# Kernel optimization log

Hardware: AMD Instinct MI355X
Metric: run time of the kernel (lower is better)

## Reference

```python
import jax, jax.numpy as jnp
import numpy as np

N, D, H, K = 131072, 512, 128, 3
NPOS, NNEG = 8192, 8192
KM_ITERS = 4
PROTO_SHIFT = 0.15
PROTO_LOGIT_SCALE = 0.2
TEMP = 2.5


def _sq_cdist(x, c):
    # squared euclidean distance, matches torch.cdist(...).pow(2)
    d = jnp.sum(x * x, -1, keepdims=True) + jnp.sum(c * c, -1)[None, :] - 2.0 * (x @ c.T)
    return jnp.maximum(d, 0.0)


def _kmeans(x, k, iters):
    # torch.linspace(0, n-1, steps=k).long() init, fixed iteration count
    n = x.shape[0]
    idx = jnp.linspace(0.0, n - 1, k).astype(jnp.int32)
    centers = x[idx]
    for _ in range(iters):
        assign = jnp.argmin(_sq_cdist(x, centers), axis=1)
        sums = jax.ops.segment_sum(x, assign, num_segments=k)
        counts = jax.ops.segment_sum(jnp.ones((n,), x.dtype), assign, num_segments=k)[:, None]
        # empty cluster keeps old center (mask.any() branch in torch)
        centers = jnp.where(counts > 0, sums / jnp.maximum(counts, 1.0), centers)
    return centers


def setup_inputs() -> dict:
    key = jax.random.key(0)
    ks = jax.random.split(key, 10)
    s = 1.0 / np.sqrt(D).astype(np.float32)
    return {
        "z_cls": jax.random.normal(ks[0], (N, D), jnp.float32),
        "z_proto": jax.random.normal(ks[1], (N, D), jnp.float32),
        "pos_ctx": jax.random.normal(ks[2], (D,), jnp.float32),
        "neg_ctx": jax.random.normal(ks[3], (D,), jnp.float32),
        "W1": jax.random.normal(ks[4], (H, D), jnp.float32) * s,
        "b1": jnp.zeros((H,), jnp.float32),
        "W2": jax.random.normal(ks[5], (1, H), jnp.float32) * (1.0 / np.sqrt(H).astype(np.float32)),
        "b2": jnp.zeros((1,), jnp.float32),
        "Wp": jax.random.normal(ks[6], (D, D), jnp.float32) * s,
        "bp": jnp.zeros((D,), jnp.float32),
        "Wn": jax.random.normal(ks[7], (D, D), jnp.float32) * s,
        "bn": jnp.zeros((D,), jnp.float32),
        "pos_idx": jax.random.randint(ks[8], (NPOS,), 0, N),
        "neg_idx": jax.random.randint(ks[9], (NNEG,), 0, N),
    }


def reference(z_cls, z_proto, pos_ctx, neg_ctx, W1, b1, W2, b2, Wp, bp, Wn, bn, pos_idx, neg_idx):
    # _build_prototypes (pos_idx/neg_idx nonempty path)
    pos_proto = _kmeans(z_proto[pos_idx], K, KM_ITERS)          # [K, D]
    neg_proto = jnp.mean(z_proto[neg_idx], axis=0)              # [D]
    # _calibrate (ema not initialized -> no EMA blend)
    pos_proto = pos_proto + PROTO_SHIFT * (pos_ctx @ Wp.T + bp)[None, :]
    neg_proto = neg_proto + PROTO_SHIFT * (neg_ctx @ Wn.T + bn)
    # distances
    d_pos_all = _sq_cdist(z_proto, pos_proto)                   # [N, K]
    d_pos = jnp.min(d_pos_all, axis=1)
    pos_assign = jnp.argmin(d_pos_all, axis=1)
    d_neg = jnp.mean((z_proto - neg_proto[None, :]) ** 2, axis=1)
    proto_logit = (d_neg - d_pos) / np.sqrt(D).astype(np.float32)
    # cls head (eval mode: dropout is identity)
    h = jax.nn.relu(z_cls @ W1.T + b1)
    cls_logit = (h @ W2.T + b2)[:, 0]
    logits = (cls_logit + PROTO_LOGIT_SCALE * proto_logit) / TEMP
    prob = jax.nn.sigmoid(logits)
    return (logits, prob, PROTO_LOGIT_SCALE * proto_logit, pos_assign, d_pos_all, pos_proto, neg_proto)
```

## Files before the change

### kernel.cpp

```cpp
#include <hip/hip_runtime.h>
#include <hip/hip_bf16.h>

#define NPTS 131072
#define DIM  512
#define HID  128
#define KCL  3
#define NPOSI 8192
#define NNEGI 8192

typedef __attribute__((ext_vector_type(8))) short bf16x8;
typedef __attribute__((ext_vector_type(4))) float f32x4;

#define ASG __attribute__((address_space(1)))
#define ASL __attribute__((address_space(3)))

enum {
  WS_SHIFT_POS = 0,
  WS_SHIFT_NEG = 512,
  WS_NEGSUM    = 1024,
  WS_NEGPART   = 1536,
  WS_SUMS      = 132608,
  WS_PPROTO    = 138764,
  WS_PN        = 140812,
  WS_W1FRAG    = 140816,
  WS_CLSL      = 173584,
};
#define SUMS_STRIDE 1539

__device__ __forceinline__ short f2bf(float x) {
  __hip_bfloat16 h = __float2bfloat16(x);
  return *reinterpret_cast<short*>(&h);
}

__global__ __launch_bounds__(256, 1) void k_prep(const float* __restrict__ W1,
                                                 const float* __restrict__ Wp, const float* __restrict__ bp,
                                                 const float* __restrict__ Wn, const float* __restrict__ bn,
                                                 const float* __restrict__ pos_ctx, const float* __restrict__ neg_ctx,
                                                 const float* __restrict__ zp, const int* __restrict__ neg_idx,
                                                 float* __restrict__ ws) {
  int bid = blockIdx.x, t = threadIdx.x;
  if (bid < 32) {
    int fid = bid * 256 + t;
    int kc = fid >> 9;
    int n  = (fid >> 6) & 7;
    int l  = fid & 63;
    int row = n * 16 + (l & 15);
    int col = kc * 32 + (l >> 4) * 8;
    const float* src = W1 + (size_t)row * DIM + col;
    float4 v0 = *(const float4*)(src);
    float4 v1 = *(const float4*)(src + 4);
    bf16x8 f;
    f[0] = f2bf(v0.x); f[1] = f2bf(v0.y); f[2] = f2bf(v0.z); f[3] = f2bf(v0.w);
    f[4] = f2bf(v1.x); f[5] = f2bf(v1.y); f[6] = f2bf(v1.z); f[7] = f2bf(v1.w);
    ((bf16x8*)(ws + WS_W1FRAG))[fid] = f;
  } else if (bid < 64) {
    int b = bid - 32;
    int mat = b >> 4;
    const float* W    = mat ? Wn : Wp;
    const float* bias = mat ? bn : bp;
    const float* ctx  = mat ? neg_ctx : pos_ctx;
    float* outp = ws + (mat ? WS_SHIFT_NEG : WS_SHIFT_POS);
    int row = (b & 15) * 32 + (t >> 3);
    int sub = t & 7;
    const float* wr = W + row * DIM + sub * 64;
    const float* cr = ctx + sub * 64;
    float s = 0.f;
#pragma unroll
    for (int j = 0; j < 64; j += 4) {
      float4 w4 = *(const float4*)(wr + j);
      float4 c4 = *(const float4*)(cr + j);
      s += w4.x * c4.x + w4.y * c4.y + w4.z * c4.z + w4.w * c4.w;
    }
    s += __shfl_xor(s, 1);
    s += __shfl_xor(s, 2);
    s += __shfl_xor(s, 4);
    if (sub == 0) outp[row] = 0.15f * (s + bias[row]);
  } else if (bid < 320) {
    int jb = bid - 64;
    int c0 = t * 2;
    float a0 = 0.f, a1 = 0.f;
    int base = jb * 32;
#pragma unroll 8
    for (int jj = 0; jj < 32; ++jj) {
      int row = neg_idx[base + jj];
      float2 v = *(const float2*)(zp + (size_t)row * DIM + c0);
      a0 += v.x; a1 += v.y;
    }
    ws[WS_NEGPART + jb * DIM + c0]     = a0;
    ws[WS_NEGPART + jb * DIM + c0 + 1] = a1;
  } else {
    for (int idx = t; idx < 4 * SUMS_STRIDE; idx += 256) ws[WS_SUMS + idx] = 0.f;
  }
}

template <int IT>
__global__ __launch_bounds__(256) void k_km(const float* __restrict__ zp,
                                            const int* __restrict__ pos_idx,
                                            float* __restrict__ ws) {
  int bid = blockIdx.x, t = threadIdx.x;
  if (IT == 0 && bid == 256) {
    int c0 = t * 2;
    float a0 = 0.f, a1 = 0.f;
#pragma unroll 8
    for (int j = 0; j < 256; ++j) {
      float2 v = *(const float2*)(ws + WS_NEGPART + j * DIM + c0);
      a0 += v.x; a1 += v.y;
    }
    ws[WS_NEGSUM + c0]     = a0;
    ws[WS_NEGSUM + c0 + 1] = a1;
    return;
  }
  __shared__ float cc[KCL * DIM];
  __shared__ float cn[KCL];
  __shared__ float lsum[KCL * DIM];
  __shared__ float lcnt[KCL];
  int w = t >> 6, l = t & 63;

  for (int idx = t; idx < KCL * DIM; idx += 256) lsum[idx] = 0.f;
  if (t < KCL) lcnt[t] = 0.f;

  for (int idx = t; idx < KCL * DIM; idx += 256) {
    int k = idx >> 9;
    int sel = (k == 0) ? 0 : ((k == 1) ? 4095 : 8191);
    float v = zp[(size_t)pos_idx[sel] * DIM + (idx & 511)];
#pragma unroll
    for (int j = 0; j < IT; ++j) {
      float cntv = ws[WS_SUMS + j * SUMS_STRIDE + 3 * DIM + k];
      float sv   = ws[WS_SUMS + j * SUMS_STRIDE + idx];
      v = (cntv > 0.f) ? sv / cntv : v;
    }
    cc[idx] = v;
  }
  __syncthreads();
  if (w < KCL) {
    float s = 0.f;
#pragma unroll
    for (int m = 0; m < 8; ++m) { float v = cc[w * DIM + l + m * 64]; s += v * v; }
#pragma unroll
    for (int m = 1; m < 64; m <<= 1) s += __shfl_xor(s, m);
    if (l == 0) cn[w] = s;
  }
  __syncthreads();

  float ck0[8], ck1[8], ck2[8];
#pragma unroll
  for (int j = 0; j < 8; ++j) {
    ck0[j] = cc[0 * DIM + l * 8 + j];
    ck1[j] = cc[1 * DIM + l * 8 + j];
    ck2[j] = cc[2 * DIM + l * 8 + j];
  }
  float cn0 = cn[0], cn1 = cn[1], cn2 = cn[2];
  float acc0[8] = {0,0,0,0,0,0,0,0}, acc1[8] = {0,0,0,0,0,0,0,0}, acc2[8] = {0,0,0,0,0,0,0,0};
  float cnt0 = 0.f, cnt1 = 0.f, cnt2 = 0.f;

  int wid = bid * 4 + w;
#pragma unroll 2
  for (int p = wid; p < NPOSI; p += 1024) {
    int row = pos_idx[p];
    const float* xr = zp + (size_t)row * DIM + l * 8;
    float4 x0 = *(const float4*)(xr);
    float4 x1 = *(const float4*)(xr + 4);
    float x[8] = {x0.x, x0.y, x0.z, x0.w, x1.x, x1.y, x1.z, x1.w};
    float d0 = 0.f, d1 = 0.f, d2 = 0.f;
#pragma unroll
    for (int j = 0; j < 8; ++j) { d0 += x[j] * ck0[j]; d1 += x[j] * ck1[j]; d2 += x[j] * ck2[j]; }
#pragma unroll
    for (int m = 1; m < 64; m <<= 1) {
      d0 += __shfl_xor(d0, m); d1 += __shfl_xor(d1, m); d2 += __shfl_xor(d2, m);
    }
    float t0 = cn0 - 2.f * d0, t1 = cn1 - 2.f * d1, t2 = cn2 - 2.f * d2;
    int a = 0; float best = t0;
    if (t1 < best) { best = t1; a = 1; }
    if (t2 < best) { best = t2; a = 2; }
    if (a == 0)      { cnt0 += 1.f;
#pragma unroll
      for (int j = 0; j < 8; ++j) acc0[j] += x[j]; }
    else if (a == 1) { cnt1 += 1.f;
#pragma unroll
      for (int j = 0; j < 8; ++j) acc1[j] += x[j]; }
    else             { cnt2 += 1.f;
#pragma unroll
      for (int j = 0; j < 8; ++j) acc2[j] += x[j]; }
  }
#pragma unroll
  for (int j = 0; j < 8; ++j) {
    atomicAdd(&lsum[0 * DIM + l * 8 + j], acc0[j]);
    atomicAdd(&lsum[1 * DIM + l * 8 + j], acc1[j]);
    atomicAdd(&lsum[2 * DIM + l * 8 + j], acc2[j]);
  }
  if (l == 0) {
    atomicAdd(&lcnt[0], cnt0); atomicAdd(&lcnt[1], cnt1); atomicAdd(&lcnt[2], cnt2);
  }
  __syncthreads();
  for (int idx = t; idx < KCL * DIM; idx += 256) atomicAdd(&ws[WS_SUMS + IT * SUMS_STRIDE + idx], lsum[idx]);
  if (t < KCL) atomicAdd(&ws[WS_SUMS + IT * SUMS_STRIDE + 3 * DIM + t], lcnt[t]);
}

__global__ __launch_bounds__(256) void k_fin(const float* __restrict__ zp,
                                             const int* __restrict__ pos_idx,
                                             float* __restrict__ ws, float* __restrict__ out) {
  __shared__ __align__(16) float pp[4 * DIM];
  int t = threadIdx.x, w = t >> 6, l = t & 63;
  for (int idx = t; idx < KCL * DIM; idx += 256) {
    int k = idx >> 9, d = idx & 511;
    int sel = (k == 0) ? 0 : ((k == 1) ? 4095 : 8191);
    float v = zp[(size_t)pos_idx[sel] * DIM + d];
#pragma unroll
    for (int j = 0; j < 4; ++j) {
      float cntv = ws[WS_SUMS + j * SUMS_STRIDE + 3 * DIM + k];
      float sv   = ws[WS_SUMS + j * SUMS_STRIDE + idx];
      v = (cntv > 0.f) ? sv / cntv : v;
    }
    pp[idx] = v + ws[WS_SHIFT_POS + d];
  }
  for (int d = t; d < DIM; d += 256)
    pp[3 * DIM + d] = ws[WS_NEGSUM + d] * (1.f / NNEGI) + ws[WS_SHIFT_NEG + d];
  __syncthreads();
  {
    float s = 0.f;
#pragma unroll
    for (int m = 0; m < 8; ++m) { float v = pp[w * DIM + l + m * 64]; s += v * v; }
#pragma unroll
    for (int m = 1; m < 64; m <<= 1) s += __shfl_xor(s, m);
    if (l == 0) ws[WS_PN + w] = s;
  }
  for (int idx = t; idx < 4 * DIM; idx += 256) {
    ws[WS_PPROTO + idx] = pp[idx];
    out[7 * NPTS + idx] = pp[idx];
  }
}

__global__ __launch_bounds__(256, 4) void k_cls(const float* __restrict__ zc,
                                                const float* __restrict__ b1,
                                                const float* __restrict__ W2,
                                                const float* __restrict__ b2,
                                                float* __restrict__ ws) {
  __shared__ __align__(16) float Azc[16 * DIM];
  __shared__ float clsv[16];

  int t = threadIdx.x, w = t >> 6, l = t & 63;
  int bid = (blockIdx.x & 7) * 1024 + (blockIdx.x >> 3);
  int i0 = bid * 16;

  {
    const float* gsrc = zc + (size_t)(i0 + w * 4) * DIM;
#pragma unroll
    for (int r = 0; r < 4; ++r) {
      int rloc = w * 4 + r;
      int swz = (rloc & 7) << 2;
#pragma unroll
      for (int seg = 0; seg < 2; ++seg) {
        int c = seg * 256 + ((l * 4) ^ swz);
        __builtin_amdgcn_global_load_lds((const ASG void*)(gsrc + (size_t)r * DIM + c),
                                         (ASL void*)&Azc[rloc * DIM + seg * 256], 16, 0, 0);
      }
    }
  }
  if (t < 16) clsv[t] = 0.f;
  int col_l = l & 15;
  float b1c[2], w2c[2];
#pragma unroll
  for (int nn = 0; nn < 2; ++nn) {
    int col = (w * 2 + nn) * 16 + col_l;
    b1c[nn] = b1[col];
    w2c[nn] = W2[col];
  }
  float b2v = b2[0];
  __syncthreads();

  {
    const bf16x8* w1f = (const bf16x8*)(ws + WS_W1FRAG);
    int sub = l >> 4, arow = l & 15;
    int swz = (arow & 7) << 2;
    int abase = arow * DIM;
    f32x4 acc[2];
    acc[0] = (f32x4){0.f, 0.f, 0.f, 0.f};
    acc[1] = (f32x4){0.f, 0.f, 0.f, 0.f};
    bf16x8 B2[3][2];
#pragma unroll
    for (int pf = 0; pf < 3; ++pf)
#pragma unroll
      for (int nn = 0; nn < 2; ++nn)
        B2[pf][nn] = w1f[pf * 512 + (w * 2 + nn) * 64 + l];

#pragma unroll
    for (int kc = 0; kc < 16; ++kc) {
      int g = kc * 32 + sub * 8;
      float4 a0 = *(const float4*)&Azc[abase + (g ^ swz)];
      float4 a1 = *(const float4*)&Azc[abase + ((g + 4) ^ swz)];
      if (kc + 3 < 16) {
#pragma unroll
        for (int nn = 0; nn < 2; ++nn)
          B2[kc % 3][nn] = w1f[(kc + 3) * 512 + (w * 2 + nn) * 64 + l];
      }
      bf16x8 af;
      af[0] = f2bf(a0.x); af[1] = f2bf(a0.y); af[2] = f2bf(a0.z); af[3] = f2bf(a0.w);
      af[4] = f2bf(a1.x); af[5] = f2bf(a1.y); af[6] = f2bf(a1.z); af[7] = f2bf(a1.w);
#pragma unroll
      for (int nn = 0; nn < 2; ++nn)
        acc[nn] = __builtin_amdgcn_mfma_f32_16x16x32_bf16(af, B2[kc % 3][nn], acc[nn], 0, 0, 0);
    }
    float prt[4] = {0.f, 0.f, 0.f, 0.f};
#pragma unroll
    for (int nn = 0; nn < 2; ++nn) {
#pragma unroll
      for (int r = 0; r < 4; ++r) {
        float h = acc[nn][r] + b1c[nn];
        h = h > 0.f ? h : 0.f;
        prt[r] += h * w2c[nn];
      }
    }
#pragma unroll
    for (int m = 1; m < 16; m <<= 1) {
#pragma unroll
      for (int r = 0; r < 4; ++r) prt[r] += __shfl_xor(prt[r], m);
    }
    if (col_l == 0) {
      float add = (w == 0) ? b2v : 0.f;
#pragma unroll
      for (int r = 0; r < 4; ++r)
        atomicAdd(&clsv[sub * 4 + r], prt[r] + add);
    }
  }
  __syncthreads();
  if (t < 16) ws[WS_CLSL + i0 + t] = clsv[t];
}

__global__ __launch_bounds__(256, 3) void k_proto(const float* __restrict__ zp,
                                                  const float* __restrict__ ws,
                                                  float* __restrict__ out) {
  __shared__ __align__(16) float Azp[16 * DIM];
  __shared__ __align__(16) float pp[4 * DIM];
  __shared__ float pns[4];

  int t = threadIdx.x, w = t >> 6, l = t & 63;
  int bid = (blockIdx.x & 7) * 1024 + (blockIdx.x >> 3);
  int i0 = bid * 16;

  {
    const float* gsrc = zp + (size_t)(i0 + w * 4) * DIM;
#pragma unroll
    for (int r = 0; r < 4; ++r) {
      int rloc = w * 4 + r;
      int swz = (rloc & 7) << 2;
#pragma unroll
      for (int seg = 0; seg < 2; ++seg) {
        int c = seg * 256 + ((l * 4) ^ swz);
        __builtin_amdgcn_global_load_lds((const ASG void*)(gsrc + (size_t)r * DIM + c),
                                         (ASL void*)&Azp[rloc * DIM + seg * 256], 16, 0, 0);
      }
    }
  }
  for (int idx = t; idx < 512; idx += 256)
    ((float4*)pp)[idx] = ((const float4*)(ws + WS_PPROTO))[idx];
  if (t < 4) pns[t] = ws[WS_PN + t];
  __syncthreads();

  int s = l & 15, r4 = l >> 4;
  int rloc = w * 4 + r4;
  int swz = (rloc & 7) << 2;
  int xbase = rloc * DIM;
  float d0 = 0.f, d1 = 0.f, d2 = 0.f, dn = 0.f, sx = 0.f;
#pragma unroll
  for (int j = 0; j < 8; ++j) {
    int c = j * 64 + s * 4;
    float4 x  = *(const float4*)&Azp[xbase + (c ^ swz)];
    float4 c0 = *(const float4*)&pp[0 * DIM + c];
    float4 c1 = *(const float4*)&pp[1 * DIM + c];
    float4 c2 = *(const float4*)&pp[2 * DIM + c];
    float4 c3 = *(const float4*)&pp[3 * DIM + c];
    d0 += x.x * c0.x + x.y * c0.y + x.z * c0.z + x.w * c0.w;
    d1 += x.x * c1.x + x.y * c1.y + x.z * c1.z + x.w * c1.w;
    d2 += x.x * c2.x + x.y * c2.y + x.z * c2.z + x.w * c2.w;
    dn += x.x * c3.x + x.y * c3.y + x.z * c3.z + x.w * c3.w;
    sx += x.x * x.x  + x.y * x.y  + x.z * x.z  + x.w * x.w;
  }
#pragma unroll
  for (int m = 1; m < 16; m <<= 1) {
    d0 += __shfl_xor(d0, m);
    d1 += __shfl_xor(d1, m);
    d2 += __shfl_xor(d2, m);
    dn += __shfl_xor(dn, m);
    sx += __shfl_xor(sx, m);
  }
  if (s == 0) {
    int i = i0 + rloc;
    float e0 = sx + pns[0] - 2.f * d0; e0 = fmaxf(e0, 0.f);
    float e1 = sx + pns[1] - 2.f * d1; e1 = fmaxf(e1, 0.f);
    float e2 = sx + pns[2] - 2.f * d2; e2 = fmaxf(e2, 0.f);
    float dpos = e0; int a = 0;
    if (e1 < dpos) { dpos = e1; a = 1; }
    if (e2 < dpos) { dpos = e2; a = 2; }
    float dneg = (sx + pns[3] - 2.f * dn) * (1.f / DIM);
    float plog = (dneg - dpos) * 0.04419417382415922f;
    float o2 = 0.2f * plog;
    float lg = (ws[WS_CLSL + i] + o2) * 0.4f;
    float prob = 1.f / (1.f + expf(-lg));
    out[i]            = lg;
    out[NPTS + i]     = prob;
    out[2 * NPTS + i] = o2;
    out[3 * NPTS + i] = (float)a;
    out[4 * NPTS + 3 * i]     = e0;
    out[4 * NPTS + 3 * i + 1] = e1;
    out[4 * NPTS + 3 * i + 2] = e2;
  }
}

extern "C" void kernel_launch(void* const* d_in, const int* in_sizes, int n_in,
                              void* d_out, int out_size, void* d_ws, size_t ws_size,
                              hipStream_t stream) {
  const float* z_cls   = (const float*)d_in[0];
  const float* z_proto = (const float*)d_in[1];
  const float* pos_ctx = (const float*)d_in[2];
  const float* neg_ctx = (const float*)d_in[3];
  const float* W1      = (const float*)d_in[4];
  const float* b1      = (const float*)d_in[5];
  const float* W2      = (const float*)d_in[6];
  const float* b2      = (const float*)d_in[7];
  const float* Wp      = (const float*)d_in[8];
  const float* bp      = (const float*)d_in[9];
  const float* Wn      = (const float*)d_in[10];
  const float* bn      = (const float*)d_in[11];
  const int* pos_idx   = (const int*)d_in[12];
  const int* neg_idx   = (const int*)d_in[13];
  float* out           = (float*)d_out;
  float* ws            = (float*)d_ws;

  k_prep<<<321, 256, 0, stream>>>(W1, Wp, bp, Wn, bn, pos_ctx, neg_ctx, z_proto, neg_idx, ws);
  k_cls<<<NPTS / 16, 256, 0, stream>>>(z_cls, b1, W2, b2, ws);
  k_km<0><<<257, 256, 0, stream>>>(z_proto, pos_idx, ws);
  k_km<1><<<256, 256, 0, stream>>>(z_proto, pos_idx, ws);
  k_km<2><<<256, 256, 0, stream>>>(z_proto, pos_idx, ws);
  k_km<3><<<256, 256, 0, stream>>>(z_proto, pos_idx, ws);
  k_fin<<<1, 256, 0, stream>>>(z_proto, pos_idx, ws, out);
  k_proto<<<NPTS / 16, 256, 0, stream>>>(z_proto, ws, out);
}
```

Baseline: 261.2 us.

## Double rows per block in cls and proto kernels, stage proto outputs in LDS

Both the classifier-head and prototype-distance kernels now process 32 rows per block instead of 16, halving the grid size. In k_cls each W1 fragment loaded from global is reused across two 16-row MFMA tiles, which halves weight-fragment traffic per row. In k_proto each wave handles two passes of rows, and outputs are staged in shared memory so they are written as contiguous coalesced runs, including the interleaved d_pos_all triples. The cost is doubled LDS per block (64KB+ for the input tile) and a lower launch-bounds occupancy target, which reduces memory latency hiding for these bandwidth-bound streaming kernels.

```diff
diff --git a/kernel.cpp b/kernel.cpp
--- a/kernel.cpp
+++ b/kernel.cpp
@@ -230,23 +230,23 @@
   }
 }
 
-__global__ __launch_bounds__(256, 4) void k_cls(const float* __restrict__ zc,
+__global__ __launch_bounds__(256, 2) void k_cls(const float* __restrict__ zc,
                                                 const float* __restrict__ b1,
                                                 const float* __restrict__ W2,
                                                 const float* __restrict__ b2,
                                                 float* __restrict__ ws) {
-  __shared__ __align__(16) float Azc[16 * DIM];
-  __shared__ float clsv[16];
+  __shared__ __align__(16) float Azc[32 * DIM];
+  __shared__ float clsv[32];
 
   int t = threadIdx.x, w = t >> 6, l = t & 63;
-  int bid = (blockIdx.x & 7) * 1024 + (blockIdx.x >> 3);
-  int i0 = bid * 16;
+  int bid = (blockIdx.x & 7) * 512 + (blockIdx.x >> 3);
+  int i0 = bid * 32;
 
   {
-    const float* gsrc = zc + (size_t)(i0 + w * 4) * DIM;
-#pragma unroll
-    for (int r = 0; r < 4; ++r) {
-      int rloc = w * 4 + r;
+    const float* gsrc = zc + (size_t)(i0 + w * 8) * DIM;
+#pragma unroll
+    for (int r = 0; r < 8; ++r) {
+      int rloc = w * 8 + r;
       int swz = (rloc & 7) << 2;
 #pragma unroll
       for (int seg = 0; seg < 2; ++seg) {
@@ -256,7 +256,7 @@
       }
     }
   }
-  if (t < 16) clsv[t] = 0.f;
+  if (t < 32) clsv[t] = 0.f;
   int col_l = l & 15;
   float b1c[2], w2c[2];
 #pragma unroll
@@ -272,10 +272,13 @@
     const bf16x8* w1f = (const bf16x8*)(ws + WS_W1FRAG);
     int sub = l >> 4, arow = l & 15;
     int swz = (arow & 7) << 2;
-    int abase = arow * DIM;
-    f32x4 acc[2];
-    acc[0] = (f32x4){0.f, 0.f, 0.f, 0.f};
-    acc[1] = (f32x4){0.f, 0.f, 0.f, 0.f};
+    int abase0 = arow * DIM;
+    int abase1 = (16 + arow) * DIM;
+    f32x4 acc[2][2];
+#pragma unroll
+    for (int rt = 0; rt < 2; ++rt)
+#pragma unroll
+      for (int nn = 0; nn < 2; ++nn) acc[rt][nn] = (f32x4){0.f, 0.f, 0.f, 0.f};
     bf16x8 B2[3][2];
 #pragma unroll
     for (int pf = 0; pf < 3; ++pf)
@@ -286,62 +289,72 @@
 #pragma unroll
     for (int kc = 0; kc < 16; ++kc) {
       int g = kc * 32 + sub * 8;
-      float4 a0 = *(const float4*)&Azc[abase + (g ^ swz)];
-      float4 a1 = *(const float4*)&Azc[abase + ((g + 4) ^ swz)];
+      float4 a00 = *(const float4*)&Azc[abase0 + (g ^ swz)];
+      float4 a01 = *(const float4*)&Azc[abase0 + ((g + 4) ^ swz)];
+      float4 a10 = *(const float4*)&Azc[abase1 + (g ^ swz)];
+      float4 a11 = *(const float4*)&Azc[abase1 + ((g + 4) ^ swz)];
       if (kc + 3 < 16) {
 #pragma unroll
         for (int nn = 0; nn < 2; ++nn)
           B2[kc % 3][nn] = w1f[(kc + 3) * 512 + (w * 2 + nn) * 64 + l];
       }
-      bf16x8 af;
-      af[0] = f2bf(a0.x); af[1] = f2bf(a0.y); af[2] = f2bf(a0.z); af[3] = f2bf(a0.w);
-      af[4] = f2bf(a1.x); af[5] = f2bf(a1.y); af[6] = f2bf(a1.z); af[7] = f2bf(a1.w);
-#pragma unroll
-      for (int nn = 0; nn < 2; ++nn)
-        acc[nn] = __builtin_amdgcn_mfma_f32_16x16x32_bf16(af, B2[kc % 3][nn], acc[nn], 0, 0, 0);
-    }
-    float prt[4] = {0.f, 0.f, 0.f, 0.f};
-#pragma unroll
-    for (int nn = 0; nn < 2; ++nn) {
-#pragma unroll
-      for (int r = 0; r < 4; ++r) {
-        float h = acc[nn][r] + b1c[nn];
-        h = h > 0.f ? h : 0.f;
-        prt[r] += h * w2c[nn];
-      }
-    }
-#pragma unroll
-    for (int m = 1; m < 16; m <<= 1) {
-#pragma unroll
-      for (int r = 0; r < 4; ++r) prt[r] += __shfl_xor(prt[r], m);
-    }
-    if (col_l == 0) {
-      float add = (w == 0) ? b2v : 0.f;
-#pragma unroll
-      for (int r = 0; r < 4; ++r)
-        atomicAdd(&clsv[sub * 4 + r], prt[r] + add);
-    }
-  }
-  __syncthreads();
-  if (t < 16) ws[WS_CLSL + i0 + t] = clsv[t];
-}
-
-__global__ __launch_bounds__(256, 3) void k_proto(const float* __restrict__ zp,
+      bf16x8 af0, af1;
+      af0[0] = f2bf(a00.x); af0[1] = f2bf(a00.y); af0[2] = f2bf(a00.z); af0[3] = f2bf(a00.w);
+      af0[4] = f2bf(a01.x); af0[5] = f2bf(a01.y); af0[6] = f2bf(a01.z); af0[7] = f2bf(a01.w);
+      af1[0] = f2bf(a10.x); af1[1] = f2bf(a10.y); af1[2] = f2bf(a10.z); af1[3] = f2bf(a10.w);
+      af1[4] = f2bf(a11.x); af1[5] = f2bf(a11.y); af1[6] = f2bf(a11.z); af1[7] = f2bf(a11.w);
+#pragma unroll
+      for (int nn = 0; nn < 2; ++nn) {
+        acc[0][nn] = __builtin_amdgcn_mfma_f32_16x16x32_bf16(af0, B2[kc % 3][nn], acc[0][nn], 0, 0, 0);
+        acc[1][nn] = __builtin_amdgcn_mfma_f32_16x16x32_bf16(af1, B2[kc % 3][nn], acc[1][nn], 0, 0, 0);
+      }
+    }
+#pragma unroll
+    for (int rt = 0; rt < 2; ++rt) {
+      float prt[4] = {0.f, 0.f, 0.f, 0.f};
+#pragma unroll
+      for (int nn = 0; nn < 2; ++nn) {
+#pragma unroll
+        for (int r = 0; r < 4; ++r) {
+          float h = acc[rt][nn][r] + b1c[nn];
+          h = h > 0.f ? h : 0.f;
+          prt[r] += h * w2c[nn];
+        }
+      }
+#pragma unroll
+      for (int m = 1; m < 16; m <<= 1) {
+#pragma unroll
+        for (int r = 0; r < 4; ++r) prt[r] += __shfl_xor(prt[r], m);
+      }
+      if (col_l == 0) {
+        float add = (w == 0) ? b2v : 0.f;
+#pragma unroll
+        for (int r = 0; r < 4; ++r)
+          atomicAdd(&clsv[rt * 16 + (l >> 4) * 4 + r], prt[r] + add);
+      }
+    }
+  }
+  __syncthreads();
+  if (t < 32) ws[WS_CLSL + i0 + t] = clsv[t];
+}
+
+__global__ __launch_bounds__(256, 2) void k_proto(const float* __restrict__ zp,
                                                   const float* __restrict__ ws,
                                                   float* __restrict__ out) {
-  __shared__ __align__(16) float Azp[16 * DIM];
+  __shared__ __align__(16) float Azp[32 * DIM];
   __shared__ __align__(16) float pp[4 * DIM];
   __shared__ float pns[4];
+  __shared__ float outst[224];
 
   int t = threadIdx.x, w = t >> 6, l = t & 63;
-  int bid = (blockIdx.x & 7) * 1024 + (blockIdx.x >> 3);
-  int i0 = bid * 16;
+  int bid = (blockIdx.x & 7) * 512 + (blockIdx.x >> 3);
+  int i0 = bid * 32;
 
   {
-    const float* gsrc = zp + (size_t)(i0 + w * 4) * DIM;
-#pragma unroll
-    for (int r = 0; r < 4; ++r) {
-      int rloc = w * 4 + r;
+    const float* gsrc = zp + (size_t)(i0 + w * 8) * DIM;
+#pragma unroll
+    for (int r = 0; r < 8; ++r) {
+      int rloc = w * 8 + r;
       int swz = (rloc & 7) << 2;
 #pragma unroll
       for (int seg = 0; seg < 2; ++seg) {
@@ -357,52 +370,64 @@
   __syncthreads();
 
   int s = l & 15, r4 = l >> 4;
-  int rloc = w * 4 + r4;
-  int swz = (rloc & 7) << 2;
-  int xbase = rloc * DIM;
-  float d0 = 0.f, d1 = 0.f, d2 = 0.f, dn = 0.f, sx = 0.f;
-#pragma unroll
-  for (int j = 0; j < 8; ++j) {
-    int c = j * 64 + s * 4;
-    float4 x  = *(const float4*)&Azp[xbase + (c ^ swz)];
-    float4 c0 = *(const float4*)&pp[0 * DIM + c];
-    float4 c1 = *(const float4*)&pp[1 * DIM + c];
-    float4 c2 = *(const float4*)&pp[2 * DIM + c];
-    float4 c3 = *(const float4*)&pp[3 * DIM + c];
-    d0 += x.x * c0.x + x.y * c0.y + x.z * c0.z + x.w * c0.w;
-    d1 += x.x * c1.x + x.y * c1.y + x.z * c1.z + x.w * c1.w;
-    d2 += x.x * c2.x + x.y * c2.y + x.z * c2.z + x.w * c2.w;
-    dn += x.x * c3.x + x.y * c3.y + x.z * c3.z + x.w * c3.w;
-    sx += x.x * x.x  + x.y * x.y  + x.z * x.z  + x.w * x.w;
-  }
-#pragma unroll
-  for (int m = 1; m < 16; m <<= 1) {
-    d0 += __shfl_xor(d0, m);
-    d1 += __shfl_xor(d1, m);
-    d2 += __shfl_xor(d2, m);
-    dn += __shfl_xor(dn, m);
-    sx += __shfl_xor(sx, m);
-  }
-  if (s == 0) {
-    int i = i0 + rloc;
-    float e0 = sx + pns[0] - 2.f * d0; e0 = fmaxf(e0, 0.f);
-    float e1 = sx + pns[1] - 2.f * d1; e1 = fmaxf(e1, 0.f);
-    float e2 = sx + pns[2] - 2.f * d2; e2 = fmaxf(e2, 0.f);
-    float dpos = e0; int a = 0;
-    if (e1 < dpos) { dpos = e1; a = 1; }
-    if (e2 < dpos) { dpos = e2; a = 2; }
-    float dneg = (sx + pns[3] - 2.f * dn) * (1.f / DIM);
-    float plog = (dneg - dpos) * 0.04419417382415922f;
-    float o2 = 0.2f * plog;
-    float lg = (ws[WS_CLSL + i] + o2) * 0.4f;
-    float prob = 1.f / (1.f + expf(-lg));
-    out[i]            = lg;
-    out[NPTS + i]     = prob;
-    out[2 * NPTS + i] = o2;
-    out[3 * NPTS + i] = (float)a;
-    out[4 * NPTS + 3 * i]     = e0;
-    out[4 * NPTS + 3 * i + 1] = e1;
-    out[4 * NPTS + 3 * i + 2] = e2;
+#pragma unroll
+  for (int pass = 0; pass < 2; ++pass) {
+    int rloc = w * 8 + pass * 4 + r4;
+    int swz = (rloc & 7) << 2;
+    int xbase = rloc * DIM;
+    float d0 = 0.f, d1 = 0.f, d2 = 0.f, dn = 0.f, sx = 0.f;
+#pragma unroll
+    for (int j = 0; j < 8; ++j) {
+      int c = j * 64 + s * 4;
+      float4 x  = *(const float4*)&Azp[xbase + (c ^ swz)];
+      float4 c0 = *(const float4*)&pp[0 * DIM + c];
+      float4 c1 = *(const float4*)&pp[1 * DIM + c];
+      float4 c2 = *(const float4*)&pp[2 * DIM + c];
+      float4 c3 = *(const float4*)&pp[3 * DIM + c];
+      d0 += x.x * c0.x + x.y * c0.y + x.z * c0.z + x.w * c0.w;
+      d1 += x.x * c1.x + x.y * c1.y + x.z * c1.z + x.w * c1.w;
+      d2 += x.x * c2.x + x.y * c2.y + x.z * c2.z + x.w * c2.w;
+      dn += x.x * c3.x + x.y * c3.y + x.z * c3.z + x.w * c3.w;
+      sx += x.x * x.x  + x.y * x.y  + x.z * x.z  + x.w * x.w;
+    }
+#pragma unroll
+    for (int m = 1; m < 16; m <<= 1) {
+      d0 += __shfl_xor(d0, m);
+      d1 += __shfl_xor(d1, m);
+      d2 += __shfl_xor(d2, m);
+      dn += __shfl_xor(dn, m);
+      sx += __shfl_xor(sx, m);
+    }
+    if (s == 0) {
+      float e0 = sx + pns[0] - 2.f * d0; e0 = fmaxf(e0, 0.f);
+      float e1 = sx + pns[1] - 2.f * d1; e1 = fmaxf(e1, 0.f);
+      float e2 = sx + pns[2] - 2.f * d2; e2 = fmaxf(e2, 0.f);
+      float dpos = e0; int a = 0;
+      if (e1 < dpos) { dpos = e1; a = 1; }
+      if (e2 < dpos) { dpos = e2; a = 2; }
+      float dneg = (sx + pns[3] - 2.f * dn) * (1.f / DIM);
+      float plog = (dneg - dpos) * 0.04419417382415922f;
+      float o2 = 0.2f * plog;
+      float lg = (ws[WS_CLSL + i0 + rloc] + o2) * 0.4f;
+      float prob = 1.f / (1.f + expf(-lg));
+      outst[rloc]       = lg;
+      outst[32 + rloc]  = prob;
+      outst[64 + rloc]  = o2;
+      outst[96 + rloc]  = (float)a;
+      outst[128 + 3 * rloc]     = e0;
+      outst[128 + 3 * rloc + 1] = e1;
+      outst[128 + 3 * rloc + 2] = e2;
+    }
+  }
+  __syncthreads();
+  if (t < 32) {
+    out[i0 + t]            = outst[t];
+    out[NPTS + i0 + t]     = outst[32 + t];
+    out[2 * NPTS + i0 + t] = outst[64 + t];
+    out[3 * NPTS + i0 + t] = outst[96 + t];
+  } else if (t >= 64 && t < 160) {
+    int u = t - 64;
+    out[4 * NPTS + 3 * i0 + u] = outst[128 + u];
   }
 }
 
@@ -427,11 +452,11 @@
   float* ws            = (float*)d_ws;
 
   k_prep<<<321, 256, 0, stream>>>(W1, Wp, bp, Wn, bn, pos_ctx, neg_ctx, z_proto, neg_idx, ws);
-  k_cls<<<NPTS / 16, 256, 0, stream>>>(z_cls, b1, W2, b2, ws);
+  k_cls<<<NPTS / 32, 256, 0, stream>>>(z_cls, b1, W2, b2, ws);
   k_km<0><<<257, 256, 0, stream>>>(z_proto, pos_idx, ws);
   k_km<1><<<256, 256, 0, stream>>>(z_proto, pos_idx, ws);
   k_km<2><<<256, 256, 0, stream>>>(z_proto, pos_idx, ws);
   k_km<3><<<256, 256, 0, stream>>>(z_proto, pos_idx, ws);
   k_fin<<<1, 256, 0, stream>>>(z_proto, pos_idx, ws, out);
-  k_proto<<<NPTS / 16, 256, 0, stream>>>(z_proto, ws, out);
-}
+  k_proto<<<NPTS / 32, 256, 0, stream>>>(z_proto, ws, out);
+}
```

Measured after the change: 290.6 us. 1.11x slower.

## Fuse cls-head tiles into k-means iteration kernels to overlap latency-bound work

Applied to the files above, without the earlier changes.

Removes the standalone cls-head kernel and splits its 8192 row tiles into four slices, each appended as extra blocks to one of the four k-means iteration launches. The small, latency-bound k-means blocks then share the GPU with bandwidth-heavy MFMA cls blocks instead of leaving most CUs idle. The cost is a larger shared-memory union buffer, a higher occupancy hint on the k-means path, and more complex block dispatch.

```diff
diff --git a/kernel.cpp b/kernel.cpp
--- a/kernel.cpp
+++ b/kernel.cpp
@@ -94,106 +94,206 @@
 }
 
 template <int IT>
-__global__ __launch_bounds__(256) void k_km(const float* __restrict__ zp,
-                                            const int* __restrict__ pos_idx,
-                                            float* __restrict__ ws) {
+__global__ __launch_bounds__(256, 4) void k_kmcls(const float* __restrict__ zp,
+                                                  const int* __restrict__ pos_idx,
+                                                  const float* __restrict__ zc,
+                                                  const float* __restrict__ b1,
+                                                  const float* __restrict__ W2,
+                                                  const float* __restrict__ b2,
+                                                  float* __restrict__ ws) {
+  __shared__ __align__(16) float Abuf[16 * DIM];
+  __shared__ float cn4[KCL + 1];
+  __shared__ float lcnt[KCL];
+  __shared__ float clsv[16];
+
   int bid = blockIdx.x, t = threadIdx.x;
-  if (IT == 0 && bid == 256) {
-    int c0 = t * 2;
-    float a0 = 0.f, a1 = 0.f;
+  int w = t >> 6, l = t & 63;
+
+  if (bid == 256) {
+    if (IT == 0) {
+      int c0 = t * 2;
+      float a0 = 0.f, a1 = 0.f;
 #pragma unroll 8
-    for (int j = 0; j < 256; ++j) {
-      float2 v = *(const float2*)(ws + WS_NEGPART + j * DIM + c0);
-      a0 += v.x; a1 += v.y;
-    }
-    ws[WS_NEGSUM + c0]     = a0;
-    ws[WS_NEGSUM + c0 + 1] = a1;
+      for (int j = 0; j < 256; ++j) {
+        float2 v = *(const float2*)(ws + WS_NEGPART + j * DIM + c0);
+        a0 += v.x; a1 += v.y;
+      }
+      ws[WS_NEGSUM + c0]     = a0;
+      ws[WS_NEGSUM + c0 + 1] = a1;
+    }
     return;
   }
-  __shared__ float cc[KCL * DIM];
-  __shared__ float cn[KCL];
-  __shared__ float lsum[KCL * DIM];
-  __shared__ float lcnt[KCL];
-  int w = t >> 6, l = t & 63;
-
-  for (int idx = t; idx < KCL * DIM; idx += 256) lsum[idx] = 0.f;
-  if (t < KCL) lcnt[t] = 0.f;
-
-  for (int idx = t; idx < KCL * DIM; idx += 256) {
-    int k = idx >> 9;
-    int sel = (k == 0) ? 0 : ((k == 1) ? 4095 : 8191);
-    float v = zp[(size_t)pos_idx[sel] * DIM + (idx & 511)];
-#pragma unroll
-    for (int j = 0; j < IT; ++j) {
-      float cntv = ws[WS_SUMS + j * SUMS_STRIDE + 3 * DIM + k];
-      float sv   = ws[WS_SUMS + j * SUMS_STRIDE + idx];
-      v = (cntv > 0.f) ? sv / cntv : v;
-    }
-    cc[idx] = v;
-  }
-  __syncthreads();
-  if (w < KCL) {
-    float s = 0.f;
-#pragma unroll
-    for (int m = 0; m < 8; ++m) { float v = cc[w * DIM + l + m * 64]; s += v * v; }
-#pragma unroll
-    for (int m = 1; m < 64; m <<= 1) s += __shfl_xor(s, m);
-    if (l == 0) cn[w] = s;
-  }
-  __syncthreads();
-
-  float ck0[8], ck1[8], ck2[8];
-#pragma unroll
-  for (int j = 0; j < 8; ++j) {
-    ck0[j] = cc[0 * DIM + l * 8 + j];
-    ck1[j] = cc[1 * DIM + l * 8 + j];
-    ck2[j] = cc[2 * DIM + l * 8 + j];
-  }
-  float cn0 = cn[0], cn1 = cn[1], cn2 = cn[2];
-  float acc0[8] = {0,0,0,0,0,0,0,0}, acc1[8] = {0,0,0,0,0,0,0,0}, acc2[8] = {0,0,0,0,0,0,0,0};
-  float cnt0 = 0.f, cnt1 = 0.f, cnt2 = 0.f;
-
-  int wid = bid * 4 + w;
+
+  if (bid < 256) {
+    float* cc   = Abuf;
+    float* lsum = Abuf + 2048;
+
+    for (int idx = t; idx < KCL * DIM; idx += 256) lsum[idx] = 0.f;
+    if (t < KCL) lcnt[t] = 0.f;
+
+    for (int idx = t; idx < KCL * DIM; idx += 256) {
+      int k = idx >> 9;
+      int sel = (k == 0) ? 0 : ((k == 1) ? 4095 : 8191);
+      float v = zp[(size_t)pos_idx[sel] * DIM + (idx & 511)];
+#pragma unroll
+      for (int j = 0; j < IT; ++j) {
+        float cntv = ws[WS_SUMS + j * SUMS_STRIDE + 3 * DIM + k];
+        float sv   = ws[WS_SUMS + j * SUMS_STRIDE + idx];
+        v = (cntv > 0.f) ? sv / cntv : v;
+      }
+      cc[idx] = v;
+    }
+    __syncthreads();
+    if (w < KCL) {
+      float s = 0.f;
+#pragma unroll
+      for (int m = 0; m < 8; ++m) { float v = cc[w * DIM + l + m * 64]; s += v * v; }
+#pragma unroll
+      for (int m = 1; m < 64; m <<= 1) s += __shfl_xor(s, m);
+      if (l == 0) cn4[w] = s;
+    }
+    __syncthreads();
+
+    float ck0[8], ck1[8], ck2[8];
+#pragma unroll
+    for (int j = 0; j < 8; ++j) {
+      ck0[j] = cc[0 * DIM + l * 8 + j];
+      ck1[j] = cc[1 * DIM + l * 8 + j];
+      ck2[j] = cc[2 * DIM + l * 8 + j];
+    }
+    float cn0 = cn4[0], cn1 = cn4[1], cn2 = cn4[2];
+    float acc0[8] = {0,0,0,0,0,0,0,0}, acc1[8] = {0,0,0,0,0,0,0,0}, acc2[8] = {0,0,0,0,0,0,0,0};
+    float cnt0 = 0.f, cnt1 = 0.f, cnt2 = 0.f;
+
+    int wid = bid * 4 + w;
 #pragma unroll 2
-  for (int p = wid; p < NPOSI; p += 1024) {
-    int row = pos_idx[p];
-    const float* xr = zp + (size_t)row * DIM + l * 8;
-    float4 x0 = *(const float4*)(xr);
-    float4 x1 = *(const float4*)(xr + 4);
-    float x[8] = {x0.x, x0.y, x0.z, x0.w, x1.x, x1.y, x1.z, x1.w};
-    float d0 = 0.f, d1 = 0.f, d2 = 0.f;
-#pragma unroll
-    for (int j = 0; j < 8; ++j) { d0 += x[j] * ck0[j]; d1 += x[j] * ck1[j]; d2 += x[j] * ck2[j]; }
-#pragma unroll
-    for (int m = 1; m < 64; m <<= 1) {
-      d0 += __shfl_xor(d0, m); d1 += __shfl_xor(d1, m); d2 += __shfl_xor(d2, m);
-    }
-    float t0 = cn0 - 2.f * d0, t1 = cn1 - 2.f * d1, t2 = cn2 - 2.f * d2;
-    int a = 0; float best = t0;
-    if (t1 < best) { best = t1; a = 1; }
-    if (t2 < best) { best = t2; a = 2; }
-    if (a == 0)      { cnt0 += 1.f;
-#pragma unroll
-      for (int j = 0; j < 8; ++j) acc0[j] += x[j]; }
-    else if (a == 1) { cnt1 += 1.f;
-#pragma unroll
-      for (int j = 0; j < 8; ++j) acc1[j] += x[j]; }
-    else             { cnt2 += 1.f;
-#pragma unroll
-      for (int j = 0; j < 8; ++j) acc2[j] += x[j]; }
-  }
-#pragma unroll
-  for (int j = 0; j < 8; ++j) {
-    atomicAdd(&lsum[0 * DIM + l * 8 + j], acc0[j]);
-    atomicAdd(&lsum[1 * DIM + l * 8 + j], acc1[j]);
-    atomicAdd(&lsum[2 * DIM + l * 8 + j], acc2[j]);
-  }
-  if (l == 0) {
-    atomicAdd(&lcnt[0], cnt0); atomicAdd(&lcnt[1], cnt1); atomicAdd(&lcnt[2], cnt2);
-  }
-  __syncthreads();
-  for (int idx = t; idx < KCL * DIM; idx += 256) atomicAdd(&ws[WS_SUMS + IT * SUMS_STRIDE + idx], lsum[idx]);
-  if (t < KCL) atomicAdd(&ws[WS_SUMS + IT * SUMS_STRIDE + 3 * DIM + t], lcnt[t]);
+    for (int p = wid; p < NPOSI; p += 1024) {
+      int row = pos_idx[p];
+      const float* xr = zp + (size_t)row * DIM + l * 8;
+      float4 x0 = *(const float4*)(xr);
+      float4 x1 = *(const float4*)(xr + 4);
+      float x[8] = {x0.x, x0.y, x0.z, x0.w, x1.x, x1.y, x1.z, x1.w};
+      float d0 = 0.f, d1 = 0.f, d2 = 0.f;
+#pragma unroll
+      for (int j = 0; j < 8; ++j) { d0 += x[j] * ck0[j]; d1 += x[j] * ck1[j]; d2 += x[j] * ck2[j]; }
+#pragma unroll
+      for (int m = 1; m < 64; m <<= 1) {
+        d0 += __shfl_xor(d0, m); d1 += __shfl_xor(d1, m); d2 += __shfl_xor(d2, m);
+      }
+      float t0 = cn0 - 2.f * d0, t1 = cn1 - 2.f * d1, t2 = cn2 - 2.f * d2;
+      int a = 0; float best = t0;
+      if (t1 < best) { best = t1; a = 1; }
+      if (t2 < best) { best = t2; a = 2; }
+      if (a == 0)      { cnt0 += 1.f;
+#pragma unroll
+        for (int j = 0; j < 8; ++j) acc0[j] += x[j]; }
+      else if (a == 1) { cnt1 += 1.f;
+#pragma unroll
+        for (int j = 0; j < 8; ++j) acc1[j] += x[j]; }
+      else             { cnt2 += 1.f;
+#pragma unroll
+        for (int j = 0; j < 8; ++j) acc2[j] += x[j]; }
+    }
+#pragma unroll
+    for (int j = 0; j < 8; ++j) {
+      atomicAdd(&lsum[0 * DIM + l * 8 + j], acc0[j]);
+      atomicAdd(&lsum[1 * DIM + l * 8 + j], acc1[j]);
+      atomicAdd(&lsum[2 * DIM + l * 8 + j], acc2[j]);
+    }
+    if (l == 0) {
+      atomicAdd(&lcnt[0], cnt0); atomicAdd(&lcnt[1], cnt1); atomicAdd(&lcnt[2], cnt2);
+    }
+    __syncthreads();
+    for (int idx = t; idx < KCL * DIM; idx += 256) atomicAdd(&ws[WS_SUMS + IT * SUMS_STRIDE + idx], lsum[idx]);
+    if (t < KCL) atomicAdd(&ws[WS_SUMS + IT * SUMS_STRIDE + 3 * DIM + t], lcnt[t]);
+    return;
+  }
+
+  {
+    int c = bid - 257;
+    int tile = IT * 2048 + ((c & 7) * 256 + (c >> 3));
+    int i0 = tile * 16;
+    float* Azc = Abuf;
+
+    const float* gsrc = zc + (size_t)(i0 + w * 4) * DIM;
+#pragma unroll
+    for (int r = 0; r < 4; ++r) {
+      int rloc = w * 4 + r;
+      int swz = (rloc & 7) << 2;
+#pragma unroll
+      for (int seg = 0; seg < 2; ++seg) {
+        int cc2 = seg * 256 + ((l * 4) ^ swz);
+        __builtin_amdgcn_global_load_lds((const ASG void*)(gsrc + (size_t)r * DIM + cc2),
+                                         (ASL void*)&Azc[rloc * DIM + seg * 256], 16, 0, 0);
+      }
+    }
+    if (t < 16) clsv[t] = 0.f;
+    int col_l = l & 15;
+    float b1c[2], w2c[2];
+#pragma unroll
+    for (int nn = 0; nn < 2; ++nn) {
+      int col = (w * 2 + nn) * 16 + col_l;
+      b1c[nn] = b1[col];
+      w2c[nn] = W2[col];
+    }
+    float b2v = b2[0];
+    __syncthreads();
+
+    const bf16x8* w1f = (const bf16x8*)(ws + WS_W1FRAG);
+    int sub = l >> 4, arow = l & 15;
+    int swz = (arow & 7) << 2;
+    int abase = arow * DIM;
+    f32x4 acc[2];
+    acc[0] = (f32x4){0.f, 0.f, 0.f, 0.f};
+    acc[1] = (f32x4){0.f, 0.f, 0.f, 0.f};
+    bf16x8 B2[3][2];
+#pragma unroll
+    for (int pf = 0; pf < 3; ++pf)
+#pragma unroll
+      for (int nn = 0; nn < 2; ++nn)
+        B2[pf][nn] = w1f[pf * 512 + (w * 2 + nn) * 64 + l];
+
+#pragma unroll
+    for (int kc = 0; kc < 16; ++kc) {
+      int g = kc * 32 + sub * 8;
+      float4 a0 = *(const float4*)&Azc[abase + (g ^ swz)];
+      float4 a1 = *(const float4*)&Azc[abase + ((g + 4) ^ swz)];
+      if (kc + 3 < 16) {
+#pragma unroll
+        for (int nn = 0; nn < 2; ++nn)
+          B2[kc % 3][nn] = w1f[(kc + 3) * 512 + (w * 2 + nn) * 64 + l];
+      }
+      bf16x8 af;
+      af[0] = f2bf(a0.x); af[1] = f2bf(a0.y); af[2] = f2bf(a0.z); af[3] = f2bf(a0.w);
+      af[4] = f2bf(a1.x); af[5] = f2bf(a1.y); af[6] = f2bf(a1.z); af[7] = f2bf(a1.w);
+#pragma unroll
+      for (int nn = 0; nn < 2; ++nn)
+        acc[nn] = __builtin_amdgcn_mfma_f32_16x16x32_bf16(af, B2[kc % 3][nn], acc[nn], 0, 0, 0);
+    }
+    float prt[4] = {0.f, 0.f, 0.f, 0.f};
+#pragma unroll
+    for (int nn = 0; nn < 2; ++nn) {
+#pragma unroll
+      for (int r = 0; r < 4; ++r) {
+        float h = acc[nn][r] + b1c[nn];
+        h = h > 0.f ? h : 0.f;
+        prt[r] += h * w2c[nn];
+      }
+    }
+#pragma unroll
+    for (int m = 1; m < 16; m <<= 1) {
+#pragma unroll
+      for (int r = 0; r < 4; ++r) prt[r] += __shfl_xor(prt[r], m);
+    }
+    if (col_l == 0) {
+      float add = (w == 0) ? b2v : 0.f;
+#pragma unroll
+      for (int r = 0; r < 4; ++r)
+        atomicAdd(&clsv[sub * 4 + r], prt[r] + add);
+    }
+    __syncthreads();
+    if (t < 16) ws[WS_CLSL + i0 + t] = clsv[t];
+  }
 }
 
 __global__ __launch_bounds__(256) void k_fin(const float* __restrict__ zp,
@@ -228,102 +328,6 @@
     ws[WS_PPROTO + idx] = pp[idx];
     out[7 * NPTS + idx] = pp[idx];
   }
-}
-
-__global__ __launch_bounds__(256, 4) void k_cls(const float* __restrict__ zc,
-                                                const float* __restrict__ b1,
-                                                const float* __restrict__ W2,
-                                                const float* __restrict__ b2,
-                                                float* __restrict__ ws) {
-  __shared__ __align__(16) float Azc[16 * DIM];
-  __shared__ float clsv[16];
-
-  int t = threadIdx.x, w = t >> 6, l = t & 63;
-  int bid = (blockIdx.x & 7) * 1024 + (blockIdx.x >> 3);
-  int i0 = bid * 16;
-
-  {
-    const float* gsrc = zc + (size_t)(i0 + w * 4) * DIM;
-#pragma unroll
-    for (int r = 0; r < 4; ++r) {
-      int rloc = w * 4 + r;
-      int swz = (rloc & 7) << 2;
-#pragma unroll
-      for (int seg = 0; seg < 2; ++seg) {
-        int c = seg * 256 + ((l * 4) ^ swz);
-        __builtin_amdgcn_global_load_lds((const ASG void*)(gsrc + (size_t)r * DIM + c),
-                                         (ASL void*)&Azc[rloc * DIM + seg * 256], 16, 0, 0);
-      }
-    }
-  }
-  if (t < 16) clsv[t] = 0.f;
-  int col_l = l & 15;
-  float b1c[2], w2c[2];
-#pragma unroll
-  for (int nn = 0; nn < 2; ++nn) {
-    int col = (w * 2 + nn) * 16 + col_l;
-    b1c[nn] = b1[col];
-    w2c[nn] = W2[col];
-  }
-  float b2v = b2[0];
-  __syncthreads();
-
-  {
-    const bf16x8* w1f = (const bf16x8*)(ws + WS_W1FRAG);
-    int sub = l >> 4, arow = l & 15;
-    int swz = (arow & 7) << 2;
-    int abase = arow * DIM;
-    f32x4 acc[2];
-    acc[0] = (f32x4){0.f, 0.f, 0.f, 0.f};
-    acc[1] = (f32x4){0.f, 0.f, 0.f, 0.f};
-    bf16x8 B2[3][2];
-#pragma unroll
-    for (int pf = 0; pf < 3; ++pf)
-#pragma unroll
-      for (int nn = 0; nn < 2; ++nn)
-        B2[pf][nn] = w1f[pf * 512 + (w * 2 + nn) * 64 + l];
-
-#pragma unroll
-    for (int kc = 0; kc < 16; ++kc) {
-      int g = kc * 32 + sub * 8;
-      float4 a0 = *(const float4*)&Azc[abase + (g ^ swz)];
-      float4 a1 = *(const float4*)&Azc[abase + ((g + 4) ^ swz)];
-      if (kc + 3 < 16) {
-#pragma unroll
-        for (int nn = 0; nn < 2; ++nn)
-          B2[kc % 3][nn] = w1f[(kc + 3) * 512 + (w * 2 + nn) * 64 + l];
-      }
-      bf16x8 af;
-      af[0] = f2bf(a0.x); af[1] = f2bf(a0.y); af[2] = f2bf(a0.z); af[3] = f2bf(a0.w);
-      af[4] = f2bf(a1.x); af[5] = f2bf(a1.y); af[6] = f2bf(a1.z); af[7] = f2bf(a1.w);
-#pragma unroll
-      for (int nn = 0; nn < 2; ++nn)
-        acc[nn] = __builtin_amdgcn_mfma_f32_16x16x32_bf16(af, B2[kc % 3][nn], acc[nn], 0, 0, 0);
-    }
-    float prt[4] = {0.f, 0.f, 0.f, 0.f};
-#pragma unroll
-    for (int nn = 0; nn < 2; ++nn) {
-#pragma unroll
-      for (int r = 0; r < 4; ++r) {
-        float h = acc[nn][r] + b1c[nn];
-        h = h > 0.f ? h : 0.f;
-        prt[r] += h * w2c[nn];
-      }
-    }
-#pragma unroll
-    for (int m = 1; m < 16; m <<= 1) {
-#pragma unroll
-      for (int r = 0; r < 4; ++r) prt[r] += __shfl_xor(prt[r], m);
-    }
-    if (col_l == 0) {
-      float add = (w == 0) ? b2v : 0.f;
-#pragma unroll
-      for (int r = 0; r < 4; ++r)
-        atomicAdd(&clsv[sub * 4 + r], prt[r] + add);
-    }
-  }
-  __syncthreads();
-  if (t < 16) ws[WS_CLSL + i0 + t] = clsv[t];
 }
 
 __global__ __launch_bounds__(256, 3) void k_proto(const float* __restrict__ zp,
@@ -427,11 +431,10 @@
   float* ws            = (float*)d_ws;
 
   k_prep<<<321, 256, 0, stream>>>(W1, Wp, bp, Wn, bn, pos_ctx, neg_ctx, z_proto, neg_idx, ws);
-  k_cls<<<NPTS / 16, 256, 0, stream>>>(z_cls, b1, W2, b2, ws);
-  k_km<0><<<257, 256, 0, stream>>>(z_proto, pos_idx, ws);
-  k_km<1><<<256, 256, 0, stream>>>(z_proto, pos_idx, ws);
-  k_km<2><<<256, 256, 0, stream>>>(z_proto, pos_idx, ws);
-  k_km<3><<<256, 256, 0, stream>>>(z_proto, pos_idx, ws);
+  k_kmcls<0><<<2305, 256, 0, stream>>>(z_proto, pos_idx, z_cls, b1, W2, b2, ws);
+  k_kmcls<1><<<2305, 256, 0, stream>>>(z_proto, pos_idx, z_cls, b1, W2, b2, ws);
+  k_kmcls<2><<<2305, 256, 0, stream>>>(z_proto, pos_idx, z_cls, b1, W2, b2, ws);
+  k_kmcls<3><<<2305, 256, 0, stream>>>(z_proto, pos_idx, z_cls, b1, W2, b2, ws);
   k_fin<<<1, 256, 0, stream>>>(z_proto, pos_idx, ws, out);
   k_proto<<<NPTS / 16, 256, 0, stream>>>(z_proto, ws, out);
 }
```

New measurement: 243.0 us (median of 2 runs). -7.0%, faster.
